# Performance work log

Hardware: AMD Instinct MI355X
Metric: run time of the kernel (lower is better)

Reference implementation:

```python
import jax, jax.numpy as jnp
import numpy as np

NEG = -1000000.0  # mask value used by the original module


def setup_inputs() -> dict:
    key = jax.random.key(0)
    ks = jax.random.split(key, 8)
    N, D_IN, D_Q, D_K, E = 8192, 512, 512, 512, 262144
    s = 1.0 / np.sqrt(D_IN)
    return {
        "x": jax.random.normal(ks[0], (N, D_IN), dtype=jnp.float32),
        "edge_index": jax.random.randint(ks[1], (2, E), 0, N, dtype=jnp.int64),
        "Wq": jax.random.normal(ks[2], (D_IN, D_Q), dtype=jnp.float32) * s,
        "bq": jax.random.normal(ks[3], (D_Q,), dtype=jnp.float32) * 0.01,
        "Wk": jax.random.normal(ks[4], (D_IN, D_K), dtype=jnp.float32) * s,
        "bk": jax.random.normal(ks[5], (D_K,), dtype=jnp.float32) * 0.01,
        "Wv": jax.random.normal(ks[6], (D_IN, D_K), dtype=jnp.float32) * s,
        "bv": jax.random.normal(ks[7], (D_K,), dtype=jnp.float32) * 0.01,
    }


def reference(x, edge_index, Wq, bq, Wk, bk, Wv, bv):
    # Linear projections (x: [N, D_in])
    q = x @ Wq + bq  # [N, Dq]
    k = x @ Wk + bk  # [N, Dk]
    v = x @ Wv + bv  # [N, Dk]

    N = x.shape[0]
    # Dense adjacency from edge list (matches torch scatter adjacency[e0, e1] = 1)
    adj = jnp.zeros((N, N), dtype=x.dtype).at[edge_index[0], edge_index[1]].set(1.0)

    # Full scores (ptr=None branch), scaled by sqrt(Dq)
    a = (q @ k.T) / jnp.sqrt(jnp.asarray(q.shape[-1], dtype=x.dtype))
    a = a * adj + (1.0 - adj) * NEG

    attn = jax.nn.softmax(a, axis=-1)  # [N, N]
    return attn @ v  # [N, Dk]
```

## Files before the change

kernel.cpp:

```cpp
#include <hip/hip_runtime.h>


#define N_NODES 8192
#define DIM 512
#define MASK_WORDS 256
#define CAPW 512
#define KV_STRIDE 1024

typedef __attribute__((ext_vector_type(8))) short short8;
typedef __attribute__((ext_vector_type(4))) float f32x4;

__device__ __forceinline__ unsigned short f2bf(float f) {
    unsigned int u = __float_as_uint(f);
    u += 0x7fffu + ((u >> 16) & 1u);
    return (unsigned short)(u >> 16);
}
__device__ __forceinline__ float bf_lo(unsigned int w) { return __uint_as_float(w << 16); }
__device__ __forceinline__ float bf_hi(unsigned int w) { return __uint_as_float(w & 0xffff0000u); }

__device__ __forceinline__ float wred_sum(float s) {
    #pragma unroll
    for (int off = 1; off <= 32; off <<= 1) s += __shfl_xor(s, off, 64);
    return s;
}
__device__ __forceinline__ int wred_sumi(int s) {
    #pragma unroll
    for (int off = 1; off <= 32; off <<= 1) s += __shfl_xor(s, off, 64);
    return s;
}
__device__ __forceinline__ float dot8(uint4 a, uint4 b) {
    return bf_lo(a.x) * bf_lo(b.x) + bf_hi(a.x) * bf_hi(b.x)
         + bf_lo(a.y) * bf_lo(b.y) + bf_hi(a.y) * bf_hi(b.y)
         + bf_lo(a.z) * bf_lo(b.z) + bf_hi(a.z) * bf_hi(b.z)
         + bf_lo(a.w) * bf_lo(b.w) + bf_hi(a.w) * bf_hi(b.w);
}

__global__ __launch_bounds__(256) void prep1(
    const float* __restrict__ x, unsigned short* __restrict__ xb,
    const float* __restrict__ Wq, const float* __restrict__ Wk,
    const float* __restrict__ Wv, unsigned short* __restrict__ Wt,
    unsigned int* __restrict__ mask)
{
    __shared__ float sm[32][33];
    const int b = blockIdx.x;
    if (b < 4096) {
        int i = b * 256 + threadIdx.x;
        float4 f = ((const float4*)x)[i];
        ushort4 o;
        o.x = f2bf(f.x); o.y = f2bf(f.y); o.z = f2bf(f.z); o.w = f2bf(f.w);
        ((ushort4*)xb)[i] = o;
        ((uint2*)mask)[i] = make_uint2(0u, 0u);
    } else {
        int bb = b - 4096;
        int which = bb >> 8, t = bb & 255;
        const float* __restrict__ W = (which == 0) ? Wq : (which == 1) ? Wk : Wv;
        unsigned short* __restrict__ outp = Wt + (size_t)which * DIM * DIM;
        int n0 = (t & 15) * 32, k0 = (t >> 4) * 32;
        int tx = threadIdx.x & 31, ty = threadIdx.x >> 5;
        #pragma unroll
        for (int r = 0; r < 4; ++r)
            sm[ty + 8 * r][tx] = W[(size_t)(k0 + ty + 8 * r) * DIM + n0 + tx];
        __syncthreads();
        #pragma unroll
        for (int r = 0; r < 4; ++r)
            outp[(size_t)(n0 + ty + 8 * r) * DIM + k0 + tx] = f2bf(sm[tx][ty + 8 * r]);
    }
}

__global__ __launch_bounds__(256) void gemm_scatter(
    const unsigned short* __restrict__ xb, const unsigned short* __restrict__ Wt,
    const float* __restrict__ bq, const float* __restrict__ bk, const float* __restrict__ bv,
    unsigned short* __restrict__ qb, unsigned short* __restrict__ kv,
    const int* __restrict__ ei, unsigned int* __restrict__ mask, int E)
{
    __shared__ unsigned short tb[64 * 128];

    const int tid = threadIdx.x;

    if (blockIdx.x >= 768) {
        int e = (blockIdx.x - 768) * 256 + tid;
        if (e < E) {
            int src = ei[e];
            int dst = ei[E + e];
            atomicOr(&mask[(size_t)src * MASK_WORDS + (dst >> 5)], 1u << (dst & 31));
        }
        return;
    }

    const int p = blockIdx.x;
    const int xcd = p & 7;
    const int s = p >> 3;
    const int mloc = s / 12;
    const int n = s - 12 * mloc;
    const int which = n >> 2;
    const int row0 = (xcd * 8 + mloc) << 7;
    const int col0 = (n & 3) << 7;

    const unsigned short* __restrict__ Bm = Wt + (size_t)which * DIM * DIM;
    const float* __restrict__ bias = (which == 0) ? bq : (which == 1) ? bk : bv;
    unsigned short* __restrict__ obase =
        (which == 0) ? qb : (which == 1) ? kv : kv + DIM;
    const size_t ostride = (which == 0) ? DIM : KV_STRIDE;

    const int lane = tid & 63;
    const int w = tid >> 6;
    const int wm = (w >> 1) * 64;
    const int wn = (w & 1) * 64;
    const int L = lane & 15;
    const int quad = lane >> 4;

    f32x4 zero = {0.f, 0.f, 0.f, 0.f};
    f32x4 acc[4][4];
    #pragma unroll
    for (int i = 0; i < 4; ++i)
        #pragma unroll
        for (int j = 0; j < 4; ++j) acc[i][j] = zero;

    const unsigned short* __restrict__ ab = xb + (size_t)(row0 + wm + L) * DIM + quad * 8;
    const unsigned short* __restrict__ bb = Bm + (size_t)(col0 + wn + L) * DIM + quad * 8;

    #pragma unroll 2
    for (int k0 = 0; k0 < DIM; k0 += 32) {
        short8 a[4], bfr[4];
        #pragma unroll
        for (int i = 0; i < 4; ++i)
            a[i] = *(const short8*)(const void*)(ab + (size_t)i * 16 * DIM + k0);
        #pragma unroll
        for (int j = 0; j < 4; ++j)
            bfr[j] = *(const short8*)(const void*)(bb + (size_t)j * 16 * DIM + k0);
        #pragma unroll
        for (int i = 0; i < 4; ++i)
            #pragma unroll
            for (int j = 0; j < 4; ++j)
                acc[i][j] = __builtin_amdgcn_mfma_f32_16x16x32_bf16(a[i], bfr[j], acc[i][j], 0, 0, 0);
    }

    float biasv[4];
    #pragma unroll
    for (int j = 0; j < 4; ++j) biasv[j] = bias[col0 + wn + j * 16 + L];

    #pragma unroll
    for (int round = 0; round < 2; ++round) {
        __syncthreads();
        if ((w >> 1) == round) {
            #pragma unroll
            for (int i = 0; i < 4; ++i)
                #pragma unroll
                for (int j = 0; j < 4; ++j)
                    #pragma unroll
                    for (int r = 0; r < 4; ++r)
                        tb[(i * 16 + quad * 4 + r) * 128 + wn + j * 16 + L] =
                            f2bf(acc[i][j][r] + biasv[j]);
        }
        __syncthreads();
        const int rrow = tid >> 2;
        const int seg = (tid & 3) * 32;
        const uint4* srcv = (const uint4*)&tb[rrow * 128 + seg];
        unsigned short* dst =
            obase + (size_t)(row0 + round * 64 + rrow) * ostride + col0 + seg;
        #pragma unroll
        for (int ss = 0; ss < 4; ++ss)
            *(uint4*)(dst + ss * 8) = srcv[ss];
    }
}

__device__ __forceinline__ void fused_pass(
    const unsigned short* __restrict__ kv,
    const unsigned short* nbrw, int cn, uint4 qv, int lane,
    float* o, float& l_run)
{
    const float scale = 0.044194173824159220f;
    for (int p0 = 0; p0 < cn; p0 += 4) {
        int j0 = nbrw[p0];
        int j1 = nbrw[(p0 + 1 < cn) ? p0 + 1 : p0];
        int j2 = nbrw[(p0 + 2 < cn) ? p0 + 2 : p0];
        int j3 = nbrw[(p0 + 3 < cn) ? p0 + 3 : p0];
        const unsigned short* n0p = kv + (size_t)j0 * KV_STRIDE + lane * 8;
        const unsigned short* n1p = kv + (size_t)j1 * KV_STRIDE + lane * 8;
        const unsigned short* n2p = kv + (size_t)j2 * KV_STRIDE + lane * 8;
        const unsigned short* n3p = kv + (size_t)j3 * KV_STRIDE + lane * 8;
        uint4 k0v = *(const uint4*)n0p;
        uint4 k1v = *(const uint4*)n1p;
        uint4 k2v = *(const uint4*)n2p;
        uint4 k3v = *(const uint4*)n3p;
        uint4 v0 = *(const uint4*)(n0p + DIM);
        uint4 v1 = *(const uint4*)(n1p + DIM);
        uint4 v2 = *(const uint4*)(n2p + DIM);
        uint4 v3 = *(const uint4*)(n3p + DIM);
        float s0 = wred_sum(dot8(qv, k0v));
        float s1 = wred_sum(dot8(qv, k1v));
        float s2 = wred_sum(dot8(qv, k2v));
        float s3 = wred_sum(dot8(qv, k3v));
        float w0 = __expf(s0 * scale);
        float w1 = (p0 + 1 < cn) ? __expf(s1 * scale) : 0.f;
        float w2 = (p0 + 2 < cn) ? __expf(s2 * scale) : 0.f;
        float w3 = (p0 + 3 < cn) ? __expf(s3 * scale) : 0.f;
        l_run += w0 + w1 + w2 + w3;
        o[0] += w0 * bf_lo(v0.x) + w1 * bf_lo(v1.x) + w2 * bf_lo(v2.x) + w3 * bf_lo(v3.x);
        o[1] += w0 * bf_hi(v0.x) + w1 * bf_hi(v1.x) + w2 * bf_hi(v2.x) + w3 * bf_hi(v3.x);
        o[2] += w0 * bf_lo(v0.y) + w1 * bf_lo(v1.y) + w2 * bf_lo(v2.y) + w3 * bf_lo(v3.y);
        o[3] += w0 * bf_hi(v0.y) + w1 * bf_hi(v1.y) + w2 * bf_hi(v2.y) + w3 * bf_hi(v3.y);
        o[4] += w0 * bf_lo(v0.z) + w1 * bf_lo(v1.z) + w2 * bf_lo(v2.z) + w3 * bf_lo(v3.z);
        o[5] += w0 * bf_hi(v0.z) + w1 * bf_hi(v1.z) + w2 * bf_hi(v2.z) + w3 * bf_hi(v3.z);
        o[6] += w0 * bf_lo(v0.w) + w1 * bf_lo(v1.w) + w2 * bf_lo(v2.w) + w3 * bf_lo(v3.w);
        o[7] += w0 * bf_hi(v0.w) + w1 * bf_hi(v1.w) + w2 * bf_hi(v2.w) + w3 * bf_hi(v3.w);
    }
}

__device__ __forceinline__ int wave_incl_scan(int pc, int lane) {
    int incl = pc;
    #pragma unroll
    for (int off = 1; off <= 32; off <<= 1) {
        int nv = __shfl_up(incl, off, 64);
        if (lane >= off) incl += nv;
    }
    return incl;
}

__global__ __launch_bounds__(256) void attn_kernel(
    const unsigned short* __restrict__ q, const unsigned short* __restrict__ kv,
    const unsigned int* __restrict__ mask, float* __restrict__ out)
{
    __shared__ unsigned short nbr[4][CAPW];

    const int tid = threadIdx.x;
    const int lane = tid & 63;
    const int wid = tid >> 6;
    const int row = blockIdx.x * 4 + wid;

    const uint4 qv = *(const uint4*)(q + (size_t)row * DIM + lane * 8);
    const unsigned int* __restrict__ mrow = mask + (size_t)row * MASK_WORDS;

    const uint4 mv = ((const uint4*)mrow)[lane];
    unsigned int wds[4] = {mv.x, mv.y, mv.z, mv.w};
    int pc = __popc(wds[0]) + __popc(wds[1]) + __popc(wds[2]) + __popc(wds[3]);
    const int total = wred_sumi(pc);

    float o[8];
    #pragma unroll
    for (int i = 0; i < 8; ++i) o[i] = 0.f;

    if (total == 0) {
        for (int j = 0; j < N_NODES; ++j) {
            uint4 vv = *(const uint4*)(kv + (size_t)j * KV_STRIDE + DIM + lane * 8);
            o[0] += bf_lo(vv.x); o[1] += bf_hi(vv.x);
            o[2] += bf_lo(vv.y); o[3] += bf_hi(vv.y);
            o[4] += bf_lo(vv.z); o[5] += bf_hi(vv.z);
            o[6] += bf_lo(vv.w); o[7] += bf_hi(vv.w);
        }
        const float sc = 1.0f / N_NODES;
        float4 r0 = {o[0] * sc, o[1] * sc, o[2] * sc, o[3] * sc};
        float4 r1 = {o[4] * sc, o[5] * sc, o[6] * sc, o[7] * sc};
        *(float4*)(out + (size_t)row * DIM + lane * 8) = r0;
        *(float4*)(out + (size_t)row * DIM + lane * 8 + 4) = r1;
        return;
    }

    float l_run = 0.f;

    if (total <= CAPW) {
        int pos = wave_incl_scan(pc, lane) - pc;
        #pragma unroll
        for (int t = 0; t < 4; ++t) {
            unsigned int ww = wds[t];
            int base = (lane * 4 + t) * 32;
            while (ww) {
                int b = __ffs(ww) - 1; ww &= ww - 1;
                nbr[wid][pos++] = (unsigned short)(base + b);
            }
        }
        fused_pass(kv, nbr[wid], total, qv, lane, o, l_run);
    } else {
        for (int c = 0; c < 16; ++c) {
            unsigned int ww = 0;
            if (lane < 16) ww = mrow[c * 16 + lane];
            int pcc = __popc(ww);
            int incl = wave_incl_scan(pcc, lane);
            int cn = __shfl(incl, 63, 64);
            if (cn == 0) continue;
            int pos = incl - pcc;
            int base = (c * 16 + lane) * 32;
            while (ww) {
                int b = __ffs(ww) - 1; ww &= ww - 1;
                nbr[wid][pos++] = (unsigned short)(base + b);
            }
            fused_pass(kv, nbr[wid], cn, qv, lane, o, l_run);
        }
    }

    const float inv = 1.0f / l_run;
    float4 r0 = {o[0] * inv, o[1] * inv, o[2] * inv, o[3] * inv};
    float4 r1 = {o[4] * inv, o[5] * inv, o[6] * inv, o[7] * inv};
    *(float4*)(out + (size_t)row * DIM + lane * 8) = r0;
    *(float4*)(out + (size_t)row * DIM + lane * 8 + 4) = r1;
}

extern "C" void kernel_launch(void* const* d_in, const int* in_sizes, int n_in,
                              void* d_out, int out_size, void* d_ws, size_t ws_size,
                              hipStream_t stream)
{
    const float* x  = (const float*)d_in[0];
    const int*   ei = (const int*)d_in[1];
    const float* Wq = (const float*)d_in[2];
    const float* bq = (const float*)d_in[3];
    const float* Wk = (const float*)d_in[4];
    const float* bk = (const float*)d_in[5];
    const float* Wv = (const float*)d_in[6];
    const float* bv = (const float*)d_in[7];
    float* out = (float*)d_out;

    const int E = in_sizes[1] / 2;
    const size_t NM = (size_t)N_NODES * DIM;

    unsigned short* xb = (unsigned short*)d_ws;
    unsigned short* Wt = xb + NM;
    unsigned short* qb = Wt + (size_t)3 * DIM * DIM;
    unsigned short* kv = qb + NM;
    unsigned int* mask = (unsigned int*)(kv + (size_t)N_NODES * KV_STRIDE);

    prep1<<<4864, 256, 0, stream>>>(x, xb, Wq, Wk, Wv, Wt, mask);

    gemm_scatter<<<768 + (E + 255) / 256, 256, 0, stream>>>(
        xb, Wt, bq, bk, bv, qb, kv, ei, mask, E);

    attn_kernel<<<N_NODES / 4, 256, 0, stream>>>(qb, kv, mask, out);
}
```

Before: 202.5 us.

## Stage projection GEMM tiles through LDS via direct global-to-LDS loads

The projection GEMM now copies 128x64 A and B tiles into shared memory with global_load_lds and has each wave read its MFMA fragments from LDS, instead of every wave loading fragments straight from global memory. The aim is to share tile data across waves and cut redundant global traffic. The epilogue drops the LDS transpose buffer and writes bf16 results directly to global memory as scattered 2-byte stores. That uncoalesced write path and the unpadded LDS layout (likely bank conflicts), with only one sync-separated stage and no double buffering, may cost more than the load sharing saves.

```diff
diff --git a/kernel.cpp b/kernel.cpp
--- a/kernel.cpp
+++ b/kernel.cpp
@@ -67,14 +67,18 @@
     }
 }
 
+__device__ __forceinline__ void load_lds16(const unsigned short* g, unsigned short* l) {
+    __builtin_amdgcn_global_load_lds(
+        (const __attribute__((address_space(1))) unsigned int*)g,
+        (__attribute__((address_space(3))) unsigned int*)l, 16, 0, 0);
+}
+
 __global__ __launch_bounds__(256) void gemm_scatter(
     const unsigned short* __restrict__ xb, const unsigned short* __restrict__ Wt,
     const float* __restrict__ bq, const float* __restrict__ bk, const float* __restrict__ bv,
     unsigned short* __restrict__ qb, unsigned short* __restrict__ kv,
     const int* __restrict__ ei, unsigned int* __restrict__ mask, int E)
 {
-    __shared__ unsigned short tb[64 * 128];
-
     const int tid = threadIdx.x;
 
     if (blockIdx.x >= 768) {
@@ -109,6 +113,9 @@
     const int L = lane & 15;
     const int quad = lane >> 4;
 
+    __shared__ unsigned short As[128 * 64];
+    __shared__ unsigned short Bs[128 * 64];
+
     f32x4 zero = {0.f, 0.f, 0.f, 0.f};
     f32x4 acc[4][4];
     #pragma unroll
@@ -116,51 +123,61 @@
         #pragma unroll
         for (int j = 0; j < 4; ++j) acc[i][j] = zero;
 
-    const unsigned short* __restrict__ ab = xb + (size_t)(row0 + wm + L) * DIM + quad * 8;
-    const unsigned short* __restrict__ bb = Bm + (size_t)(col0 + wn + L) * DIM + quad * 8;
-
-    #pragma unroll 2
-    for (int k0 = 0; k0 < DIM; k0 += 32) {
-        short8 a[4], bfr[4];
-        #pragma unroll
-        for (int i = 0; i < 4; ++i)
-            a[i] = *(const short8*)(const void*)(ab + (size_t)i * 16 * DIM + k0);
-        #pragma unroll
-        for (int j = 0; j < 4; ++j)
-            bfr[j] = *(const short8*)(const void*)(bb + (size_t)j * 16 * DIM + k0);
-        #pragma unroll
-        for (int i = 0; i < 4; ++i)
+    int sm_[4], sg_[4];
+    #pragma unroll
+    for (int t = 0; t < 4; ++t) {
+        int c = tid + t * 256;
+        sm_[t] = c >> 3;
+        sg_[t] = (c & 7) << 3;
+    }
+    const unsigned short* __restrict__ arow = xb + (size_t)row0 * DIM;
+    const unsigned short* __restrict__ brow = Bm + (size_t)col0 * DIM;
+
+    for (int k0 = 0; k0 < DIM; k0 += 64) {
+        #pragma unroll
+        for (int t = 0; t < 4; ++t)
+            load_lds16(arow + (size_t)sm_[t] * DIM + k0 + sg_[t], As + (tid + t * 256) * 8);
+        #pragma unroll
+        for (int t = 0; t < 4; ++t)
+            load_lds16(brow + (size_t)sm_[t] * DIM + k0 + sg_[t], Bs + (tid + t * 256) * 8);
+        __syncthreads();
+
+        short8 a[2][4], bfr[2][4];
+        #pragma unroll
+        for (int kk = 0; kk < 2; ++kk) {
+            #pragma unroll
+            for (int i = 0; i < 4; ++i)
+                a[kk][i] = *(const short8*)(const void*)
+                    &As[(wm + i * 16 + L) * 64 + kk * 32 + quad * 8];
             #pragma unroll
             for (int j = 0; j < 4; ++j)
-                acc[i][j] = __builtin_amdgcn_mfma_f32_16x16x32_bf16(a[i], bfr[j], acc[i][j], 0, 0, 0);
-    }
-
-    float biasv[4];
-    #pragma unroll
-    for (int j = 0; j < 4; ++j) biasv[j] = bias[col0 + wn + j * 16 + L];
-
-    #pragma unroll
-    for (int round = 0; round < 2; ++round) {
-        __syncthreads();
-        if ((w >> 1) == round) {
+                bfr[kk][j] = *(const short8*)(const void*)
+                    &Bs[(wn + j * 16 + L) * 64 + kk * 32 + quad * 8];
+        }
+        #pragma unroll
+        for (int kk = 0; kk < 2; ++kk)
             #pragma unroll
             for (int i = 0; i < 4; ++i)
                 #pragma unroll
                 for (int j = 0; j < 4; ++j)
-                    #pragma unroll
-                    for (int r = 0; r < 4; ++r)
-                        tb[(i * 16 + quad * 4 + r) * 128 + wn + j * 16 + L] =
-                            f2bf(acc[i][j][r] + biasv[j]);
-        }
+                    acc[i][j] = __builtin_amdgcn_mfma_f32_16x16x32_bf16(
+                        a[kk][i], bfr[kk][j], acc[i][j], 0, 0, 0);
         __syncthreads();
-        const int rrow = tid >> 2;
-        const int seg = (tid & 3) * 32;
-        const uint4* srcv = (const uint4*)&tb[rrow * 128 + seg];
-        unsigned short* dst =
-            obase + (size_t)(row0 + round * 64 + rrow) * ostride + col0 + seg;
-        #pragma unroll
-        for (int ss = 0; ss < 4; ++ss)
-            *(uint4*)(dst + ss * 8) = srcv[ss];
+    }
+
+    float biasv[4];
+    #pragma unroll
+    for (int j = 0; j < 4; ++j) biasv[j] = bias[col0 + wn + j * 16 + L];
+    #pragma unroll
+    for (int i = 0; i < 4; ++i) {
+        int r0 = row0 + wm + i * 16 + quad * 4;
+        #pragma unroll
+        for (int j = 0; j < 4; ++j) {
+            int c = col0 + wn + j * 16 + L;
+            #pragma unroll
+            for (int r = 0; r < 4; ++r)
+                obase[(size_t)(r0 + r) * ostride + c] = f2bf(acc[i][j][r] + biasv[j]);
+        }
     }
 }
 
```

Result: faster. 172.2 us (-14.9%).
